# Optimization experiments

Hardware: AMD Instinct MI355X
Metric: run time of the kernel (lower is better)

The kernel has to match this reference:

```python
import jax, jax.numpy as jnp
import numpy as np

B = 8192
K = 40          # history blocks of 61
STATS = 383     # 99 base + 120 + 10 + 150 + 4 option dims
D = 165 + 61 * K + STATS  # 2988


def _mha(q, k, v, kpm, w_in, b_in, w_out, b_out, nh=4):
    """PyTorch nn.MultiheadAttention (batch_first) math. kpm: True = masked key."""
    Bq, Lq, E = q.shape
    hd = E // nh
    wq, wk, wv = jnp.split(w_in, 3, axis=0)
    bq, bk, bv = jnp.split(b_in, 3)
    qh = (q @ wq.T + bq).reshape(Bq, Lq, nh, hd).transpose(0, 2, 1, 3)
    kh = (k @ wk.T + bk).reshape(Bq, -1, nh, hd).transpose(0, 2, 1, 3)
    vh = (v @ wv.T + bv).reshape(Bq, -1, nh, hd).transpose(0, 2, 1, 3)
    s = jnp.einsum('bhqd,bhkd->bhqk', qh, kh) * jnp.float32(1.0 / np.sqrt(hd))
    if kpm is not None:
        s = jnp.where(kpm[:, None, None, :], jnp.float32(-1e9), s)
    a = jax.nn.softmax(s, axis=-1)
    o = jnp.einsum('bhqk,bhkd->bhqd', a, vh).transpose(0, 2, 1, 3).reshape(Bq, Lq, E)
    return o @ w_out.T + b_out


def _ln(x, g, b, eps=1e-5):
    m = x.mean(-1, keepdims=True)
    v = ((x - m) ** 2).mean(-1, keepdims=True)
    return (x - m) / jnp.sqrt(v + eps) * g + b


def setup_inputs() -> dict:
    key = jax.random.key(0)
    ks = iter(jax.random.split(key, 64))
    def p(shape, scale=0.02):
        return jax.random.normal(next(ks), shape, dtype=jnp.float32) * scale
    return {
        'obs': jax.random.normal(next(ks), (B, D), dtype=jnp.float32),
        'seat_team_vec': jax.random.normal(next(ks), (B, 6), dtype=jnp.float32),
        'card_emb': p((40, 32)),
        'w_cnt_hand': p((16, 3)), 'b_cnt_hand': p((16,)),
        'w_cnt_cap': p((16, 2)), 'b_cnt_cap': p((16,)),
        'h2t_win': p((96, 32)), 'h2t_bin': p((96,)), 'h2t_wout': p((32, 32)), 'h2t_bout': p((32,)),
        't2h_win': p((96, 32)), 't2h_bin': p((96,)), 't2h_wout': p((32, 32)), 't2h_bout': p((32,)),
        'w_merge': p((64, 224)), 'b_merge': p((64,)),
        'w_hproj': p((64, 61)), 'b_hproj': p((64,)),
        'pos_emb': p((40, 64)),
        'enc_win': p((192, 64)), 'enc_bin': p((192,)), 'enc_wout': p((64, 64)), 'enc_bout': p((64,)),
        'ln1_g': jnp.ones((64,), jnp.float32), 'ln1_b': jnp.zeros((64,), jnp.float32),
        'w_ff1': p((128, 64)), 'b_ff1': p((128,)),
        'w_ff2': p((64, 128)), 'b_ff2': p((64,)),
        'ln2_g': jnp.ones((64,), jnp.float32), 'ln2_b': jnp.zeros((64,), jnp.float32),
        'w_stats': p((64, STATS)), 'b_stats': p((64,)),
        'w_seat': p((32, 6)), 'b_seat': p((32,)),
        'w_comb': p((256, 224)), 'b_comb': p((256,)),
    }


def reference(obs, seat_team_vec, card_emb, w_cnt_hand, b_cnt_hand, w_cnt_cap, b_cnt_cap,
              h2t_win, h2t_bin, h2t_wout, h2t_bout, t2h_win, t2h_bin, t2h_wout, t2h_bout,
              w_merge, b_merge, w_hproj, b_hproj, pos_emb,
              enc_win, enc_bin, enc_wout, enc_bout, ln1_g, ln1_b,
              w_ff1, b_ff1, w_ff2, b_ff2, ln2_g, ln2_b,
              w_stats, b_stats, w_seat, b_seat, w_comb, b_comb):
    Bn = obs.shape[0]
    k = K  # static: decoded from D = 165 + 61*K + STATS
    hand_table = obs[:, :83]
    captured = obs[:, 83:165]
    history = obs[:, 165:165 + 61 * k]
    stats = obs[:, 165 + 61 * k:]

    hand_mask = hand_table[:, :40]
    other_counts = hand_table[:, 40:43]
    table_mask = hand_table[:, 43:83]

    hand_feat = hand_mask @ card_emb      # [B,32]
    table_feat = table_mask @ card_emb
    other_cnt_feat = jax.nn.relu(other_counts @ w_cnt_hand.T + b_cnt_hand)

    hand_present = hand_mask > 0.5
    table_present = table_mask > 0.5
    hand_seq = hand_mask[:, :, None] * card_emb    # [B,40,32]
    table_seq = table_mask[:, :, None] * card_emb

    # _safe_mha: rows whose keys are all padded produce zeros
    h2t = _mha(hand_seq, table_seq, table_seq, ~table_present, h2t_win, h2t_bin, h2t_wout, h2t_bout)
    h2t = jnp.where(table_present.any(axis=1)[:, None, None], h2t, jnp.float32(0.0))
    t2h = _mha(table_seq, hand_seq, hand_seq, ~hand_present, t2h_win, t2h_bin, t2h_wout, t2h_bout)
    t2h = jnp.where(hand_present.any(axis=1)[:, None, None], t2h, jnp.float32(0.0))

    def masked_mean(x, present):
        m = present[:, :, None].astype(x.dtype)
        return (x * m).sum(1) / jnp.maximum(m.sum(1), 1.0)
    hand_attn_feat = masked_mean(h2t, hand_present)
    table_attn_feat = masked_mean(t2h, table_present)

    cap0_feat = captured[:, :40] @ card_emb
    cap1_feat = captured[:, 40:80] @ card_emb
    cap_cnt_feat = jax.nn.relu(captured[:, 80:82] @ w_cnt_cap.T + b_cnt_cap)

    set_merged = jnp.concatenate([hand_feat, table_feat, cap0_feat, cap1_feat,
                                  hand_attn_feat, table_attn_feat,
                                  other_cnt_feat, cap_cnt_feat], axis=1)  # [B,224]
    set_feat = jax.nn.relu(set_merged @ w_merge.T + b_merge)              # [B,64]

    # 1-layer post-norm TransformerEncoder (eval mode, no dropout)
    hseq = history.reshape(Bn, k, 61) @ w_hproj.T + b_hproj + pos_emb[:k]  # [B,k,64]
    sa = _mha(hseq, hseq, hseq, None, enc_win, enc_bin, enc_wout, enc_bout)
    x = _ln(hseq + sa, ln1_g, ln1_b)
    ff = jax.nn.relu(x @ w_ff1.T + b_ff1) @ w_ff2.T + b_ff2
    x = _ln(x + ff, ln2_g, ln2_b)
    hist_feat = x.mean(axis=1)                                            # [B,64]

    stats_feat = jax.nn.relu(stats @ w_stats.T + b_stats)                 # [B,64]
    seat_feat = jax.nn.relu(seat_team_vec @ w_seat.T + b_seat)            # [B,32]

    combined = jnp.concatenate([set_feat, hist_feat, stats_feat, seat_feat], axis=1)  # [B,224]
    return jax.nn.relu(combined @ w_comb.T + b_comb)                      # [B,256]
```

## Files before the change

kernel.cpp:

```cpp
#include <hip/hip_runtime.h>

#define TPB 512

#define OFF_CV      0
#define OFF_POSB    2560
#define OFF_G       3840
#define OFF_U       10240
#define OFF_V       10560
#define OFF_CTB     10880
#define OFF_FRHP    10888
#define OFF_FRAG    14984
#define FR_QKV      0
#define FR_OUT      12288
#define FR_FF1      16384
#define FR_FF2      24576
#define OFF_ONES    47752
#define OFF_MERGE   48264
#define OFF_STATS   62600
#define OFF_COMB    74856
#define OFF_WO2     132200
#define WS_TOTAL    133224

#define SA_OFF    0
#define HISTH_OFF 10240
#define HISTL_OFF 16768
#define QPL_OFF   10240
#define KF_OFF    16384
#define KZ_OFF    22528
#define OH_OFF    10240
#define FF1P_OFF  10240
#define DH_OFF    23296
#define DL_OFF    30208
#define P_OFF     23296
#define YTAIL_OFF 36096
#define Z_OFF     37120
#define VF_OFF    37120
#define SHT_OFF   47360
#define SOM_OFF   48032
#define SSM_OFF   48544
#define SCB_OFF   49440
#define R12_OFF   50464
#define SCNT_OFF  52512
#define SMEM_BYTES 52520

typedef __attribute__((ext_vector_type(8))) short bf16x8;
typedef __attribute__((ext_vector_type(4))) float f32x4;

struct P {
  const float *obs, *seat, *ce, *wch, *bch, *wcc, *bcc,
    *h2t_win, *h2t_bin, *h2t_wout, *h2t_bout,
    *t2h_win, *t2h_bin, *t2h_wout, *t2h_bout,
    *w_merge, *b_merge, *w_hproj, *b_hproj, *pos,
    *enc_win, *enc_bin, *enc_wout, *enc_bout,
    *ln1_g, *ln1_b, *w_ff1, *b_ff1, *w_ff2, *b_ff2, *ln2_g, *ln2_b,
    *w_stats, *b_stats, *w_seat, *b_seat, *w_comb, *b_comb;
  const float* ws;
  float* out;
};

__device__ __host__ inline unsigned bfpack(float a, float b, int plane) {
  unsigned ua = __float_as_uint(a) & 0xFFFF0000u;
  unsigned ub = __float_as_uint(b) & 0xFFFF0000u;
  if (plane == 0) return (ua >> 16) | ub;
  float ra = a - __uint_as_float(ua), rb = b - __uint_as_float(ub);
  return (__float_as_uint(ra) >> 16) | (__float_as_uint(rb) & 0xFFFF0000u);
}

__device__ __host__ inline unsigned short bf16rne(float x) {
  unsigned u = __float_as_uint(x);
  return (unsigned short)((u + 0x7FFFu + ((u >> 16) & 1u)) >> 16);
}

__device__ __host__ inline unsigned packrne(float a, float b) {
  return (unsigned)bf16rne(a) | ((unsigned)bf16rne(b) << 16);
}

__device__ inline float bf_lo(unsigned u) { return __uint_as_float(u << 16); }
__device__ inline float bf_hi(unsigned u) { return __uint_as_float(u & 0xFFFF0000u); }

__device__ inline bf16x8 ld_b64x2(const char* pp) {
  bf16x8 v;
  *((uint2*)&v) = *(const uint2*)(pp);
  *(((uint2*)&v) + 1) = *(const uint2*)(pp + 8);
  return v;
}

#define CSCALE 0.35355339059327373f

__global__ void prep_kernel(P p, float* ws) {
  int t = blockIdx.x * blockDim.x + threadIdx.x;
  if (t >= WS_TOTAL) return;
  unsigned* wsu = (unsigned*)ws;
  if (t < OFF_POSB) {
    int a = t / 1280, rem = t - a * 1280;
    int i = rem >> 5, d = rem & 31;
    const float* win = a ? p.t2h_win : p.h2t_win;
    const float* wr = win + (64 + d) * 32;
    const float* cr = p.ce + i * 32;
    float acc = 0.f;
    #pragma unroll
    for (int j = 0; j < 32; ++j) acc += cr[j] * wr[j];
    ws[t] = acc;
  } else if (t < OFF_G) {
    int r = t - OFF_POSB; int i = r >> 5, u = r & 31;
    float a = p.b_hproj[2 * u] + p.pos[i * 64 + 2 * u];
    float b = p.b_hproj[2 * u + 1] + p.pos[i * 64 + 2 * u + 1];
    wsu[t] = packrne(a, b);
  } else if (t < OFF_U) {
    int r = t - OFF_G;
    int u = r % 20; int i = (r / 20) % 40; int h = (r / 800) & 3; int a = r / 3200;
    const float* win = a ? p.t2h_win : p.h2t_win;
    const float* cri = p.ce + i * 32;
    float g2[2];
    #pragma unroll
    for (int half = 0; half < 2; ++half) {
      int j = 2 * u + half;
      const float* crj = p.ce + j * 32;
      float g = 0.f;
      for (int e = 0; e < 8; ++e) {
        const float* wq = win + (h * 8 + e) * 32;
        const float* wk = win + (32 + h * 8 + e) * 32;
        float pq = 0.f, pk = 0.f;
        for (int m = 0; m < 32; ++m) { pq += cri[m] * wq[m]; pk += crj[m] * wk[m]; }
        g += pq * pk;
      }
      g2[half] = g * CSCALE;
    }
    wsu[t] = packrne(g2[0], g2[1]);
  } else if (t < OFF_V) {
    int r = t - OFF_U; int i = r % 40; int h = (r / 40) & 3; int a = r / 160;
    const float* win = a ? p.t2h_win : p.h2t_win;
    const float* bin = a ? p.t2h_bin : p.h2t_bin;
    const float* cri = p.ce + i * 32;
    float u = 0.f;
    for (int e = 0; e < 8; ++e) {
      const float* wq = win + (h * 8 + e) * 32;
      float pq = 0.f;
      for (int m = 0; m < 32; ++m) pq += cri[m] * wq[m];
      u += pq * bin[32 + h * 8 + e];
    }
    ws[t] = u * CSCALE;
  } else if (t < OFF_CTB) {
    int r = t - OFF_V; int j = r % 40; int h = (r / 40) & 3; int a = r / 160;
    const float* win = a ? p.t2h_win : p.h2t_win;
    const float* bin = a ? p.t2h_bin : p.h2t_bin;
    const float* crj = p.ce + j * 32;
    float v = 0.f;
    for (int e = 0; e < 8; ++e) {
      const float* wk = win + (32 + h * 8 + e) * 32;
      float pk = 0.f;
      for (int m = 0; m < 32; ++m) pk += crj[m] * wk[m];
      v += pk * bin[h * 8 + e];
    }
    ws[t] = v * CSCALE;
  } else if (t < OFF_FRHP) {
    int r = t - OFF_CTB; int h = r & 3; int a = r >> 2;
    const float* bin = a ? p.t2h_bin : p.h2t_bin;
    float c = 0.f;
    for (int e = 0; e < 8; ++e) c += bin[h * 8 + e] * bin[32 + h * 8 + e];
    ws[t] = c * CSCALE;
  } else if (t < OFF_FRAG) {
    int r = t - OFF_FRHP;
    int plane = r >> 11; r &= 2047; int kt = r >> 10; r &= 1023;
    int nt = r >> 8; r &= 255; int lane = r >> 2; int u = r & 3;
    int k = kt * 32 + (lane >> 4) * 8 + u * 2;
    int n = nt * 16 + (lane & 15);
    float a = (k < 61) ? p.w_hproj[n * 61 + k] : 0.f;
    float b = (k + 1 < 61) ? p.w_hproj[n * 61 + k + 1] : 0.f;
    wsu[t] = bfpack(a, b, plane);
  } else if (t < OFF_ONES) {
    int r = t - OFF_FRAG;
    int plane, kt, nt, lane, u;
    const float* src; int ldk;
    if (r < FR_OUT) {
      plane = r / 6144; r %= 6144; kt = r / 3072; r %= 3072;
      nt = r >> 8; r &= 255; lane = r >> 2; u = r & 3;
      src = p.enc_win; ldk = 64;
    } else if (r < FR_FF1) {
      r -= FR_OUT; plane = r >> 11; r &= 2047; kt = r >> 10; r &= 1023;
      nt = r >> 8; r &= 255; lane = r >> 2; u = r & 3;
      src = p.enc_wout; ldk = 64;
    } else if (r < FR_FF2) {
      r -= FR_FF1; plane = r >> 12; r &= 4095; kt = r >> 11; r &= 2047;
      nt = r >> 8; r &= 255; lane = r >> 2; u = r & 3;
      src = p.w_ff1; ldk = 64;
    } else {
      r -= FR_FF2; plane = r >> 12; r &= 4095; kt = r >> 10; r &= 1023;
      nt = r >> 8; r &= 255; lane = r >> 2; u = r & 3;
      src = p.w_ff2; ldk = 128;
    }
    int k = kt * 32 + (lane >> 4) * 8 + u * 2;
    int n = nt * 16 + (lane & 15);
    float a = src[n * ldk + k], b = src[n * ldk + k + 1];
    wsu[t] = bfpack(a, b, plane);
  } else if (t < OFF_MERGE) {
    int r = t - OFF_ONES;
    int kt = r >> 8, rr = r & 255;
    int lane = rr >> 2, u = rr & 3;
    int k = kt * 32 + (lane >> 4) * 8 + u * 2;
    wsu[t] = ((k < 40) ? 0x00003F80u : 0u) | ((k + 1 < 40) ? 0x3F800000u : 0u);
  } else if (t < OFF_STATS) {
    int r = t - OFF_MERGE; int j = r >> 6, d = r & 63;
    ws[t] = p.w_merge[d * 224 + j];
  } else if (t < OFF_COMB) {
    int r = t - OFF_STATS;
    int j = r >> 5, pp = r & 31;
    wsu[t] = packrne(p.w_stats[(2 * pp) * 383 + j], p.w_stats[(2 * pp + 1) * 383 + j]);
  } else if (t < OFF_WO2) {
    int r = t - OFF_COMB;
    int jq = r >> 10, rem = r & 1023;
    int n = rem >> 2, c = rem & 3;
    ws[t] = p.w_comb[n * 224 + jq * 4 + c];
  } else {
    int r = t - OFF_WO2; int a = r >> 9; int rr = r & 511;
    int e = rr >> 4, u = rr & 15;
    const float* src = a ? p.t2h_wout : p.h2t_wout;
    wsu[t] = packrne(src[(2 * u) * 32 + e], src[(2 * u + 1) * 32 + e]);
  }
}

#define FMA4(acc, a4, w0, w1, w2, w3)                                   \
  acc.x += a4.x * w0.x + a4.y * w1.x + a4.z * w2.x + a4.w * w3.x;       \
  acc.y += a4.x * w0.y + a4.y * w1.y + a4.z * w2.y + a4.w * w3.y;       \
  acc.z += a4.x * w0.z + a4.y * w1.z + a4.z * w2.z + a4.w * w3.z;       \
  acc.w += a4.x * w0.w + a4.y * w1.w + a4.z * w2.w + a4.w * w3.w;

#define MFMA16(acc, a, b) acc = __builtin_amdgcn_mfma_f32_16x16x32_bf16(a, b, acc, 0, 0, 0)

__global__ __launch_bounds__(TPB, 3) void enc_row(P p) {
  const int row = blockIdx.x;
  const int tid = threadIdx.x;
  const int lane = tid & 63, wq = tid >> 6;
  const int lane15 = lane & 15, lg = lane >> 4;

  __shared__ unsigned smem_u[SMEM_BYTES / 4];
  char* smem = (char*)smem_u;
  float* sA   = (float*)(smem + SA_OFF);
  float* sZ   = (float*)(smem + Z_OFF);
  float* s_ht = (float*)(smem + SHT_OFF);
  float* s_om = (float*)(smem + SOM_OFF);
  float* s_sm = (float*)(smem + SSM_OFF);
  float* s_cb = (float*)(smem + SCB_OFF);
  float* s_r12 = (float*)(smem + R12_OFF);
  int*   s_cnt = (int*)(smem + SCNT_OFF);

  const float* orow = p.obs + (size_t)row * 2988;
  const float* ws = p.ws;
  const unsigned* wsu = (const unsigned*)ws;

  if (tid < 165) s_ht[tid] = orow[tid];
  if (tid < 256) ((unsigned*)(smem + YTAIL_OFF))[tid] = 0u;
  if (tid < 256) {
    int feat = tid >> 6, q = tid & 63;
    int d = q >> 1, jh = q & 1;
    const int offs[4] = {0, 43, 83, 123};
    const int dsts[4] = {0, 32, 64, 96};
    int off = offs[feat];
    float a = 0.f;
    for (int j = jh * 20; j < jh * 20 + 20; ++j)
      a += orow[off + j] * p.ce[j * 32 + d];
    float other = __shfl_xor(a, 1, 64);
    if (jh == 0) s_sm[dsts[feat] + d] = a + other;
  } else if (tid < 272) {
    int d = tid - 256;
    float a = p.bch[d];
    for (int j = 0; j < 3; ++j) a += orow[40 + j] * p.wch[d * 3 + j];
    s_sm[192 + d] = fmaxf(a, 0.f);
  } else if (tid < 288) {
    int d = tid - 272;
    float a = p.bcc[d];
    for (int j = 0; j < 2; ++j) a += orow[163 + j] * p.wcc[d * 2 + j];
    s_sm[208 + d] = fmaxf(a, 0.f);
  } else if (tid < 352) {
    s_sm[128 + tid - 288] = 0.f;
  } else if (tid < 480) {
    s_om[tid - 352] = 0.f;
  } else if (tid == 480) {
    int c = 0; for (int i = 0; i < 40; ++i) c += (orow[i] > 0.5f);
    s_cnt[0] = c;
  } else if (tid == 481) {
    int c = 0; for (int i = 0; i < 40; ++i) c += (orow[43 + i] > 0.5f);
    s_cnt[1] = c;
  }
  if (tid < 64) s_cb[128 + tid] = p.b_stats[tid];
  else if (tid < 128) s_cb[tid - 64] = p.b_merge[tid - 64];
  else if (tid < 256) s_r12[tid - 128] = 0.f;
  for (int m = tid; m < 2560; m += TPB) {
    int i = m >> 6, j = m & 63;
    float val = (j < 61) ? orow[165 + i * 61 + j] : 0.f;
    unsigned hb = __float_as_uint(val) & 0xFFFF0000u;
    *(unsigned short*)(smem + HISTH_OFF + i * 136 + j * 2) = (unsigned short)(hb >> 16);
    float rr = val - __uint_as_float(hb);
    *(unsigned short*)(smem + HISTL_OFF + i * 136 + j * 2) =
        (unsigned short)(__float_as_uint(rr) >> 16);
  }
  for (int m = tid; m < 2560; m += TPB) sZ[m] = ws[OFF_CV + m];
  __syncthreads();
  #define OB(i) s_ht[i]

  for (int t = wq; t < 12; t += 8) {
    int rt = t % 3, nt = t / 3;
    int n = nt * 16 + lane15;
    int arow = rt * 16 + lane15;
    f32x4 acc;
    #pragma unroll
    for (int r = 0; r < 4; ++r) {
      int i = rt * 16 + lg * 4 + r;
      if (i < 40) {
        unsigned pb = wsu[OFF_POSB + i * 32 + (n >> 1)];
        acc[r] = (n & 1) ? bf_hi(pb) : bf_lo(pb);
      } else acc[r] = 0.f;
    }
    #pragma unroll
    for (int kt = 0; kt < 2; ++kt) {
      int kb = kt * 32 + lg * 8;
      bf16x8 aH = ld_b64x2(smem + HISTH_OFF + arow * 136 + kb * 2);
      bf16x8 aL = ld_b64x2(smem + HISTL_OFF + arow * 136 + kb * 2);
      bf16x8 bH = *(const bf16x8*)(wsu + OFF_FRHP + kt * 1024 + nt * 256 + lane * 4);
      bf16x8 bL = *(const bf16x8*)(wsu + OFF_FRHP + 2048 + kt * 1024 + nt * 256 + lane * 4);
      MFMA16(acc, aH, bH); MFMA16(acc, aH, bL); MFMA16(acc, aL, bH);
    }
    #pragma unroll
    for (int r = 0; r < 4; ++r) {
      int i = rt * 16 + lg * 4 + r;
      if (i < 40) {
        sA[i * 64 + n] = acc[r];
        unsigned hb = __float_as_uint(acc[r]) & 0xFFFF0000u;
        *(unsigned short*)(smem + DH_OFF + i * 144 + n * 2) = (unsigned short)(hb >> 16);
        float rr = acc[r] - __uint_as_float(hb);
        *(unsigned short*)(smem + DL_OFF + i * 144 + n * 2) =
            (unsigned short)(__float_as_uint(rr) >> 16);
      }
    }
  }
  if (tid < 320) {
    int a = tid / 160, r = tid - a * 160;
    int h = r / 40, i = r - h * 40;
    int qoff = a ? 43 : 0, koff = a ? 0 : 43;
    float qm = OB(qoff + i);
    const unsigned* Gp = wsu + OFF_G + ((a * 4 + h) * 40 + i) * 20;
    const float* vp = ws + OFF_V + (a * 4 + h) * 40;
    const float* Cv = sZ + a * 1280;
    const float* bin = a ? p.t2h_bin : p.h2t_bin;
    float base = ws[OFF_CTB + a * 4 + h] + qm * ws[OFF_U + (a * 4 + h) * 40 + i];
    const int e0 = h * 8;
    float den = 0.f;
    float o0 = 0.f, o1 = 0.f, o2 = 0.f, o3 = 0.f;
    float o4 = 0.f, o5 = 0.f, o6 = 0.f, o7 = 0.f;
    for (int j = 0; j < 40; ++j) {
      float km = OB(koff + j);
      if (km > 0.5f) {
        unsigned g2 = Gp[j >> 1];
        float gj = (j & 1) ? bf_hi(g2) : bf_lo(g2);
        float s = fmaf(km, fmaf(qm, gj, vp[j]), base);
        float pj = __expf(s);
        den += pj;
        float pk = pj * km;
        float4 v0 = *(const float4*)(Cv + j * 32 + e0);
        float4 v1 = *(const float4*)(Cv + j * 32 + e0 + 4);
        o0 += pk * v0.x; o1 += pk * v0.y; o2 += pk * v0.z; o3 += pk * v0.w;
        o4 += pk * v1.x; o5 += pk * v1.y; o6 += pk * v1.z; o7 += pk * v1.w;
      }
    }
    if (qm > 0.5f) {
      float inv = 1.f / den;
      float4 bv0 = *(const float4*)(bin + 64 + e0);
      float4 bv1 = *(const float4*)(bin + 64 + e0 + 4);
      float* om = s_om + (i & 1) * 64 + a * 32 + e0;
      atomicAdd(&om[0], o0 * inv + bv0.x);
      atomicAdd(&om[1], o1 * inv + bv0.y);
      atomicAdd(&om[2], o2 * inv + bv0.z);
      atomicAdd(&om[3], o3 * inv + bv0.w);
      atomicAdd(&om[4], o4 * inv + bv1.x);
      atomicAdd(&om[5], o5 * inv + bv1.y);
      atomicAdd(&om[6], o6 * inv + bv1.z);
      atomicAdd(&om[7], o7 * inv + bv1.w);
    }
  } else {
    int r = tid - 320;
    int c = r >> 4, d0 = (r & 15) << 2;
    int j0 = c << 5, j1 = (c == 11) ? 383 : j0 + 32;
    const float* st = orow + 2605;
    const unsigned* wt = wsu + OFF_STATS + (d0 >> 1);
    float x0 = 0.f, x1 = 0.f, x2 = 0.f, x3 = 0.f;
    for (int j = j0; j < j1; ++j) {
      float a0 = st[j];
      unsigned u0 = wt[j * 32], u1 = wt[j * 32 + 1];
      x0 += a0 * bf_lo(u0); x1 += a0 * bf_hi(u0);
      x2 += a0 * bf_lo(u1); x3 += a0 * bf_hi(u1);
    }
    float* bank = (c & 1) ? s_r12 : (s_cb + 128);
    atomicAdd(&bank[d0 + 0], x0);
    atomicAdd(&bank[d0 + 1], x1);
    atomicAdd(&bank[d0 + 2], x2);
    atomicAdd(&bank[d0 + 3], x3);
  }
  __syncthreads();

  for (int t = wq; t < 36; t += 8) {
    int rt = t % 3, nt = t / 3;
    int n = nt * 16 + lane15;
    int arow = rt * 16 + lane15;
    float bia = p.enc_bin[n];
    f32x4 acc = {bia, bia, bia, bia};
    #pragma unroll
    for (int kt = 0; kt < 2; ++kt) {
      int kb = kt * 32 + lg * 8;
      bf16x8 aH = *(const bf16x8*)(smem + DH_OFF + arow * 144 + kb * 2);
      bf16x8 aL = *(const bf16x8*)(smem + DL_OFF + arow * 144 + kb * 2);
      bf16x8 bH = *(const bf16x8*)(wsu + OFF_FRAG + FR_QKV + kt * 3072 + nt * 256 + lane * 4);
      bf16x8 bL = *(const bf16x8*)(wsu + OFF_FRAG + FR_QKV + 6144 + kt * 3072 + nt * 256 + lane * 4);
      MFMA16(acc, aH, bH); MFMA16(acc, aH, bL); MFMA16(acc, aL, bH);
    }
    if (nt < 4) {
      #pragma unroll
      for (int r = 0; r < 4; ++r) {
        int i = rt * 16 + lg * 4 + r;
        if (i < 40)
          *(unsigned short*)(smem + QPL_OFF + ((nt * 48 + i) * 16 + lane15) * 2) =
              bf16rne(acc[r]);
      }
    } else if (nt < 8) {
      int h = nt - 4, e = lane15;
      int lp = (e >> 3) << 4, us = e & 7;
      #pragma unroll
      for (int r = 0; r < 4; ++r) {
        int j = rt * 16 + lg * 4 + r;
        if (j < 40) {
          int lanep = lp + (j & 15);
          *(unsigned short*)(smem + KF_OFF +
              (((h * 3 + (j >> 4)) * 32 + lanep) * 8 + us) * 2) = bf16rne(acc[r]);
        }
      }
    } else {
      int h = nt - 8, e = lane15;
      #pragma unroll
      for (int r = 0; r < 4; ++r) {
        int j = rt * 16 + lg * 4 + r;
        if (j < 40) {
          int kt = j >> 5, k_ = j & 31;
          int lanep = ((k_ >> 3) << 4) | e;
          *(unsigned short*)(smem + VF_OFF +
              (((h * 2 + kt) * 64 + lanep) * 8 + (k_ & 7)) * 2) = bf16rne(acc[r]);
        }
      }
    }
  }
  if (tid < 128) ((unsigned*)(smem + KZ_OFF))[tid] = 0u;
  for (int m = tid; m < 768; m += TPB) {
    int h = m / 192, rem = m - h * 192;
    ((unsigned*)(smem + VF_OFF))[(h * 2 + 1) * 256 + 64 + rem] = 0u;
  }
  if (tid >= 448 && tid < 480) {
    int r = tid - 448;
    int a = r >> 4, q = r & 15;
    int d0 = (q >> 1) << 2, eh = q & 1;
    int ch = s_cnt[0], ct = s_cnt[1];
    if (ch > 0 && ct > 0) {
      float ic = 1.f / (float)(a ? ct : ch);
      const unsigned* wt = wsu + OFF_WO2 + a * 512 + (d0 >> 1);
      float4 v = make_float4(0.f, 0.f, 0.f, 0.f);
      if (eh == 0) v = *(const float4*)((a ? p.t2h_bout : p.h2t_bout) + d0);
      for (int e = eh * 16; e < eh * 16 + 16; ++e) {
        float oe = (s_om[a * 32 + e] + s_om[64 + a * 32 + e]) * ic;
        unsigned w01 = wt[e * 16], w23 = wt[e * 16 + 1];
        v.x += oe * bf_lo(w01); v.y += oe * bf_hi(w01);
        v.z += oe * bf_lo(w23); v.w += oe * bf_hi(w23);
      }
      atomicAdd(&s_sm[128 + a * 32 + d0 + 0], v.x);
      atomicAdd(&s_sm[128 + a * 32 + d0 + 1], v.y);
      atomicAdd(&s_sm[128 + a * 32 + d0 + 2], v.z);
      atomicAdd(&s_sm[128 + a * 32 + d0 + 3], v.w);
    }
  }
  __syncthreads();

  for (int t = wq; t < 36; t += 8) {
    int h = t / 9, rr = t % 9;
    int rt = rr / 3, nt = rr % 3;
    int arow = rt * 16 + lane15;
    f32x4 acc = {0.f, 0.f, 0.f, 0.f};
    bf16x8 aH = *(const bf16x8*)(smem + QPL_OFF + ((h * 48 + arow) * 16 + (lg & 1) * 8) * 2);
    int boff = (lane < 32) ? (KF_OFF + (((h * 3 + nt) * 32 + lane) * 8) * 2)
                           : (KZ_OFF + ((lane & 31) * 8) * 2);
    bf16x8 bH = *(const bf16x8*)(smem + boff);
    MFMA16(acc, aH, bH);
    int j = nt * 16 + lane15;
    if (j < 40) {
      #pragma unroll
      for (int r = 0; r < 4; ++r) {
        int i = rt * 16 + lg * 4 + r;
        if (i < 40)
          *(unsigned short*)(smem + P_OFF + h * 3200 + i * 80 + j * 2) =
              bf16rne(__expf(acc[r] * 0.25f));
      }
    }
  }
  __syncthreads();

  {
    bf16x8 ones0 = *(const bf16x8*)(wsu + OFF_ONES + lane * 4);
    bf16x8 ones1 = *(const bf16x8*)(wsu + OFF_ONES + 256 + lane * 4);
    for (int t = wq; t < 12; t += 8) {
      int h = t / 3, rt = t % 3;
      int arow = rt * 16 + lane15;
      const char* pb = smem + P_OFF + h * 3200 + arow * 80;
      bf16x8 a0 = *(const bf16x8*)(pb + lg * 16);
      bf16x8 a1 = {0, 0, 0, 0, 0, 0, 0, 0};
      if (lg == 0) a1 = *(const bf16x8*)(pb + 64);
      bf16x8 v0 = *(const bf16x8*)(smem + VF_OFF + ((h * 2 + 0) * 64 + lane) * 16);
      bf16x8 v1 = *(const bf16x8*)(smem + VF_OFF + ((h * 2 + 1) * 64 + lane) * 16);
      f32x4 accV = {0.f, 0.f, 0.f, 0.f}, accD = {0.f, 0.f, 0.f, 0.f};
      MFMA16(accV, a0, v0); MFMA16(accV, a1, v1);
      MFMA16(accD, a0, ones0); MFMA16(accD, a1, ones1);
      #pragma unroll
      for (int r = 0; r < 4; ++r) {
        int i = rt * 16 + lg * 4 + r;
        if (i < 40) {
          float o = accV[r] / accD[r];
          *(unsigned short*)(smem + OH_OFF + (i * 72 + h * 16 + lane15) * 2) =
              bf16rne(o);
        }
      }
    }
  }
  if (tid >= 256 && tid < 384) {
    int r = tid - 256;
    int d0 = (r & 15) << 2, jc = r >> 4;
    const float* wt = ws + OFF_MERGE + d0;
    float4 acc = make_float4(0.f, 0.f, 0.f, 0.f);
    int j0 = jc * 28;
    for (int j = j0; j < j0 + 28; j += 4) {
      float4 a4 = *(const float4*)(s_sm + j);
      float4 w0 = *(const float4*)(wt + j * 64);
      float4 w1 = *(const float4*)(wt + (j + 1) * 64);
      float4 w2 = *(const float4*)(wt + (j + 2) * 64);
      float4 w3 = *(const float4*)(wt + (j + 3) * 64);
      FMA4(acc, a4, w0, w1, w2, w3);
    }
    float* bank = (jc & 1) ? (s_r12 + 64) : s_cb;
    atomicAdd(&bank[d0 + 0], acc.x);
    atomicAdd(&bank[d0 + 1], acc.y);
    atomicAdd(&bank[d0 + 2], acc.z);
    atomicAdd(&bank[d0 + 3], acc.w);
  }
  __syncthreads();

  for (int t = wq; t < 12; t += 8) {
    int rt = t % 3, nt = t / 3;
    int n = nt * 16 + lane15;
    int arow = rt * 16 + lane15;
    f32x4 acc;
    #pragma unroll
    for (int r = 0; r < 4; ++r) {
      int i = rt * 16 + lg * 4 + r;
      acc[r] = p.enc_bout[n] + ((i < 40) ? sA[i * 64 + n] : 0.f);
    }
    #pragma unroll
    for (int kt = 0; kt < 2; ++kt) {
      int kb = kt * 32 + lg * 8;
      bf16x8 aH = *(const bf16x8*)(smem + OH_OFF + arow * 144 + kb * 2);
      bf16x8 bH = *(const bf16x8*)(wsu + OFF_FRAG + FR_OUT + kt * 1024 + nt * 256 + lane * 4);
      bf16x8 bL = *(const bf16x8*)(wsu + OFF_FRAG + FR_OUT + 2048 + kt * 1024 + nt * 256 + lane * 4);
      MFMA16(acc, aH, bH); MFMA16(acc, aH, bL);
    }
    #pragma unroll
    for (int r = 0; r < 4; ++r) {
      int i = rt * 16 + lg * 4 + r;
      if (i < 40) sZ[i * 64 + n] = acc[r];
    }
  }
  __syncthreads();

  {
    float g = p.ln1_g[lane], b = p.ln1_b[lane];
    for (int i = wq; i < 40; i += 8) {
      float x = sZ[(i << 6) + lane];
      float s = x;
      #pragma unroll
      for (int off = 32; off; off >>= 1) s += __shfl_xor(s, off, 64);
      float m = s * 0.015625f;
      float xm = x - m;
      float v = xm * xm;
      #pragma unroll
      for (int off = 32; off; off >>= 1) v += __shfl_xor(v, off, 64);
      float rs = rsqrtf(v * 0.015625f + 1e-5f);
      float val = xm * rs * g + b;
      sA[(i << 6) + lane] = val;
      unsigned hb = __float_as_uint(val) & 0xFFFF0000u;
      *(unsigned short*)(smem + DH_OFF + i * 144 + lane * 2) = (unsigned short)(hb >> 16);
      float rr = val - __uint_as_float(hb);
      *(unsigned short*)(smem + DL_OFF + i * 144 + lane * 2) =
          (unsigned short)(__float_as_uint(rr) >> 16);
    }
  }
  __syncthreads();

  for (int t = wq; t < 24; t += 8) {
    int rt = t % 3, nt = t / 3;
    int n = nt * 16 + lane15;
    int arow = rt * 16 + lane15;
    float bia = p.b_ff1[n];
    f32x4 acc = {bia, bia, bia, bia};
    #pragma unroll
    for (int kt = 0; kt < 2; ++kt) {
      int kb = kt * 32 + lg * 8;
      bf16x8 aH = *(const bf16x8*)(smem + DH_OFF + arow * 144 + kb * 2);
      bf16x8 aL = *(const bf16x8*)(smem + DL_OFF + arow * 144 + kb * 2);
      bf16x8 bH = *(const bf16x8*)(wsu + OFF_FRAG + FR_FF1 + kt * 2048 + nt * 256 + lane * 4);
      bf16x8 bL = *(const bf16x8*)(wsu + OFF_FRAG + FR_FF1 + 4096 + kt * 2048 + nt * 256 + lane * 4);
      MFMA16(acc, aH, bH); MFMA16(acc, aH, bL); MFMA16(acc, aL, bH);
    }
    #pragma unroll
    for (int r = 0; r < 4; ++r) {
      int i = rt * 16 + lg * 4 + r;
      float v = fmaxf(acc[r], 0.f);
      *(unsigned short*)(smem + FF1P_OFF + i * 272 + n * 2) = bf16rne(v);
    }
  }
  __syncthreads();

  for (int t = wq; t < 12; t += 8) {
    int rt = t % 3, nt = t / 3;
    int n = nt * 16 + lane15;
    int arow = rt * 16 + lane15;
    f32x4 acc;
    #pragma unroll
    for (int r = 0; r < 4; ++r) {
      int i = rt * 16 + lg * 4 + r;
      acc[r] = p.b_ff2[n] + ((i < 40) ? sA[i * 64 + n] : 0.f);
    }
    #pragma unroll
    for (int kt = 0; kt < 4; ++kt) {
      int kb = kt * 32 + lg * 8;
      bf16x8 aH = *(const bf16x8*)(smem + FF1P_OFF + arow * 272 + kb * 2);
      bf16x8 bH = *(const bf16x8*)(wsu + OFF_FRAG + FR_FF2 + kt * 1024 + nt * 256 + lane * 4);
      bf16x8 bL = *(const bf16x8*)(wsu + OFF_FRAG + FR_FF2 + 4096 + kt * 1024 + nt * 256 + lane * 4);
      MFMA16(acc, aH, bH); MFMA16(acc, aH, bL);
    }
    #pragma unroll
    for (int r = 0; r < 4; ++r) {
      int i = rt * 16 + lg * 4 + r;
      if (i < 40) sZ[i * 64 + n] = acc[r];
    }
  }
  __syncthreads();

  {
    float g = p.ln2_g[lane], b = p.ln2_b[lane];
    for (int i = wq; i < 40; i += 8) {
      float x = sZ[(i << 6) + lane];
      float s = x;
      #pragma unroll
      for (int off = 32; off; off >>= 1) s += __shfl_xor(s, off, 64);
      float m = s * 0.015625f;
      float xm = x - m;
      float v = xm * xm;
      #pragma unroll
      for (int off = 32; off; off >>= 1) v += __shfl_xor(v, off, 64);
      float rs = rsqrtf(v * 0.015625f + 1e-5f);
      sA[(i << 6) + lane] = xm * rs * g + b;
    }
  }
  __syncthreads();

  if (tid < 64) {
    float a = 0.f;
    for (int i = 0; i < 40; ++i) a += sA[(i << 6) + tid];
    s_cb[64 + tid] = a * 0.025f;
    s_cb[128 + tid] = fmaxf(s_cb[128 + tid] + s_r12[tid], 0.f);
    s_cb[tid] = fmaxf(s_cb[tid] + s_r12[64 + tid], 0.f);
  } else if (tid < 96) {
    int d = tid - 64;
    const float* sv = p.seat + (size_t)row * 6;
    float acc = p.b_seat[d];
    for (int j = 0; j < 6; ++j) acc += sv[j] * p.w_seat[d * 6 + j];
    s_cb[192 + d] = fmaxf(acc, 0.f);
  }
  __syncthreads();

  {
    int n = tid & 255, half = tid >> 8;
    const float* wt = ws + OFF_COMB + n * 4;
    float acc = half ? 0.f : p.b_comb[n];
    int jq0 = half * 28;
    for (int jq = jq0; jq < jq0 + 28; ++jq) {
      float4 a4 = *(const float4*)(s_cb + jq * 4);
      float4 w = *(const float4*)(wt + jq * 1024);
      acc += a4.x * w.x + a4.y * w.y + a4.z * w.z + a4.w * w.w;
    }
    s_r12[half * 256 + n] = acc;
  }
  __syncthreads();
  if (tid < 256)
    p.out[(size_t)row * 256 + tid] = fmaxf(s_r12[tid] + s_r12[256 + tid], 0.f);
  #undef OB
}

extern "C" void kernel_launch(void* const* d_in, const int* in_sizes, int n_in,
                              void* d_out, int out_size, void* d_ws, size_t ws_size,
                              hipStream_t stream) {
  typedef const float* F;
  P p;
  p.obs      = (F)d_in[0];
  p.seat     = (F)d_in[1];
  p.ce       = (F)d_in[2];
  p.wch      = (F)d_in[3];
  p.bch      = (F)d_in[4];
  p.wcc      = (F)d_in[5];
  p.bcc      = (F)d_in[6];
  p.h2t_win  = (F)d_in[7];
  p.h2t_bin  = (F)d_in[8];
  p.h2t_wout = (F)d_in[9];
  p.h2t_bout = (F)d_in[10];
  p.t2h_win  = (F)d_in[11];
  p.t2h_bin  = (F)d_in[12];
  p.t2h_wout = (F)d_in[13];
  p.t2h_bout = (F)d_in[14];
  p.w_merge  = (F)d_in[15];
  p.b_merge  = (F)d_in[16];
  p.w_hproj  = (F)d_in[17];
  p.b_hproj  = (F)d_in[18];
  p.pos      = (F)d_in[19];
  p.enc_win  = (F)d_in[20];
  p.enc_bin  = (F)d_in[21];
  p.enc_wout = (F)d_in[22];
  p.enc_bout = (F)d_in[23];
  p.ln1_g    = (F)d_in[24];
  p.ln1_b    = (F)d_in[25];
  p.w_ff1    = (F)d_in[26];
  p.b_ff1    = (F)d_in[27];
  p.w_ff2    = (F)d_in[28];
  p.b_ff2    = (F)d_in[29];
  p.ln2_g    = (F)d_in[30];
  p.ln2_b    = (F)d_in[31];
  p.w_stats  = (F)d_in[32];
  p.b_stats  = (F)d_in[33];
  p.w_seat   = (F)d_in[34];
  p.b_seat   = (F)d_in[35];
  p.w_comb   = (F)d_in[36];
  p.b_comb   = (F)d_in[37];
  p.ws  = (const float*)d_ws;
  p.out = (float*)d_out;

  const int Bn = in_sizes[0] / 2988;
  hipLaunchKernelGGL(prep_kernel, dim3((WS_TOTAL + 255) / 256), dim3(256), 0, stream,
                     p, (float*)d_ws);
  hipLaunchKernelGGL(enc_row, dim3(Bn), dim3(TPB), 0, stream, p);
}
```

Measured before the change: 825.4 us.

## Shrink shared memory with bf16 activations to fit four blocks per CU

Stores the residual/LN activation buffers sA and sZ as bf16 instead of fp32. It also reads the Cv table straight from global memory instead of staging it in LDS, and drops the zero-padding buffers (YTAIL, KZ) by zeroing the B operand in registers. Shared memory shrinks from about 52KB to about 41KB and launch bounds rise to 4 blocks per CU, aiming for higher occupancy. The cost is lower precision on the residual path and LayerNorm outputs, plus extra global reads for Cv.

```diff
diff --git a/kernel.cpp b/kernel.cpp
--- a/kernel.cpp
+++ b/kernel.cpp
@@ -22,26 +22,25 @@
 #define WS_TOTAL    133224
 
 #define SA_OFF    0
-#define HISTH_OFF 10240
-#define HISTL_OFF 16768
-#define QPL_OFF   10240
-#define KF_OFF    16384
-#define KZ_OFF    22528
-#define OH_OFF    10240
-#define FF1P_OFF  10240
-#define DH_OFF    23296
-#define DL_OFF    30208
-#define P_OFF     23296
-#define YTAIL_OFF 36096
-#define Z_OFF     37120
-#define VF_OFF    37120
-#define SHT_OFF   47360
-#define SOM_OFF   48032
-#define SSM_OFF   48544
-#define SCB_OFF   49440
-#define R12_OFF   50464
-#define SCNT_OFF  52512
-#define SMEM_BYTES 52520
+#define HISTH_OFF 5120
+#define HISTL_OFF 10560
+#define QPL_OFF   5120
+#define KF_OFF    10240
+#define OH_OFF    5120
+#define FF1P_OFF  5120
+#define DH_OFF    16384
+#define DL_OFF    22144
+#define P_OFF     16384
+#define Z_OFF     29184
+#define VF_OFF    29184
+#define BNK_OFF   37376
+#define SHT_OFF   37888
+#define SOM_OFF   38548
+#define SSM_OFF   39060
+#define SCB_OFF   39956
+#define SCNT_OFF  40852
+#define R12_OFF   37888
+#define SMEM_BYTES 40860
 
 typedef __attribute__((ext_vector_type(8))) short bf16x8;
 typedef __attribute__((ext_vector_type(4))) float f32x4;
@@ -77,6 +76,9 @@
 
 __device__ inline float bf_lo(unsigned u) { return __uint_as_float(u << 16); }
 __device__ inline float bf_hi(unsigned u) { return __uint_as_float(u & 0xFFFF0000u); }
+__device__ inline float bfus(unsigned short u) {
+  return __uint_as_float(((unsigned)u) << 16);
+}
 
 __device__ inline bf16x8 ld_b64x2(const char* pp) {
   bf16x8 v;
@@ -227,7 +229,7 @@
 
 #define MFMA16(acc, a, b) acc = __builtin_amdgcn_mfma_f32_16x16x32_bf16(a, b, acc, 0, 0, 0)
 
-__global__ __launch_bounds__(TPB, 3) void enc_row(P p) {
+__global__ __launch_bounds__(TPB, 4) void enc_row(P p) {
   const int row = blockIdx.x;
   const int tid = threadIdx.x;
   const int lane = tid & 63, wq = tid >> 6;
@@ -235,12 +237,13 @@
 
   __shared__ unsigned smem_u[SMEM_BYTES / 4];
   char* smem = (char*)smem_u;
-  float* sA   = (float*)(smem + SA_OFF);
-  float* sZ   = (float*)(smem + Z_OFF);
-  float* s_ht = (float*)(smem + SHT_OFF);
-  float* s_om = (float*)(smem + SOM_OFF);
-  float* s_sm = (float*)(smem + SSM_OFF);
-  float* s_cb = (float*)(smem + SCB_OFF);
+  unsigned short* sAu = (unsigned short*)(smem + SA_OFF);
+  unsigned short* sZu = (unsigned short*)(smem + Z_OFF);
+  float* s_bnk = (float*)(smem + BNK_OFF);
+  float* s_ht  = (float*)(smem + SHT_OFF);
+  float* s_om  = (float*)(smem + SOM_OFF);
+  float* s_sm  = (float*)(smem + SSM_OFF);
+  float* s_cb  = (float*)(smem + SCB_OFF);
   float* s_r12 = (float*)(smem + R12_OFF);
   int*   s_cnt = (int*)(smem + SCNT_OFF);
 
@@ -249,7 +252,6 @@
   const unsigned* wsu = (const unsigned*)ws;
 
   if (tid < 165) s_ht[tid] = orow[tid];
-  if (tid < 256) ((unsigned*)(smem + YTAIL_OFF))[tid] = 0u;
   if (tid < 256) {
     int feat = tid >> 6, q = tid & 63;
     int d = q >> 1, jh = q & 1;
@@ -284,7 +286,7 @@
   }
   if (tid < 64) s_cb[128 + tid] = p.b_stats[tid];
   else if (tid < 128) s_cb[tid - 64] = p.b_merge[tid - 64];
-  else if (tid < 256) s_r12[tid - 128] = 0.f;
+  else if (tid < 256) s_bnk[tid - 128] = 0.f;
   for (int m = tid; m < 2560; m += TPB) {
     int i = m >> 6, j = m & 63;
     float val = (j < 61) ? orow[165 + i * 61 + j] : 0.f;
@@ -294,7 +296,6 @@
     *(unsigned short*)(smem + HISTL_OFF + i * 136 + j * 2) =
         (unsigned short)(__float_as_uint(rr) >> 16);
   }
-  for (int m = tid; m < 2560; m += TPB) sZ[m] = ws[OFF_CV + m];
   __syncthreads();
   #define OB(i) s_ht[i]
 
@@ -324,7 +325,7 @@
     for (int r = 0; r < 4; ++r) {
       int i = rt * 16 + lg * 4 + r;
       if (i < 40) {
-        sA[i * 64 + n] = acc[r];
+        sAu[i * 64 + n] = bf16rne(acc[r]);
         unsigned hb = __float_as_uint(acc[r]) & 0xFFFF0000u;
         *(unsigned short*)(smem + DH_OFF + i * 144 + n * 2) = (unsigned short)(hb >> 16);
         float rr = acc[r] - __uint_as_float(hb);
@@ -340,7 +341,7 @@
     float qm = OB(qoff + i);
     const unsigned* Gp = wsu + OFF_G + ((a * 4 + h) * 40 + i) * 20;
     const float* vp = ws + OFF_V + (a * 4 + h) * 40;
-    const float* Cv = sZ + a * 1280;
+    const float* Cv = ws + OFF_CV + a * 1280;
     const float* bin = a ? p.t2h_bin : p.h2t_bin;
     float base = ws[OFF_CTB + a * 4 + h] + qm * ws[OFF_U + (a * 4 + h) * 40 + i];
     const int e0 = h * 8;
@@ -389,7 +390,7 @@
       x0 += a0 * bf_lo(u0); x1 += a0 * bf_hi(u0);
       x2 += a0 * bf_lo(u1); x3 += a0 * bf_hi(u1);
     }
-    float* bank = (c & 1) ? s_r12 : (s_cb + 128);
+    float* bank = (c & 1) ? s_bnk : (s_cb + 128);
     atomicAdd(&bank[d0 + 0], x0);
     atomicAdd(&bank[d0 + 1], x1);
     atomicAdd(&bank[d0 + 2], x2);
@@ -417,7 +418,7 @@
       for (int r = 0; r < 4; ++r) {
         int i = rt * 16 + lg * 4 + r;
         if (i < 40)
-          *(unsigned short*)(smem + QPL_OFF + ((nt * 48 + i) * 16 + lane15) * 2) =
+          *(unsigned short*)(smem + QPL_OFF + ((nt * 40 + i) * 16 + lane15) * 2) =
               bf16rne(acc[r]);
       }
     } else if (nt < 8) {
@@ -446,7 +447,6 @@
       }
     }
   }
-  if (tid < 128) ((unsigned*)(smem + KZ_OFF))[tid] = 0u;
   for (int m = tid; m < 768; m += TPB) {
     int h = m / 192, rem = m - h * 192;
     ((unsigned*)(smem + VF_OFF))[(h * 2 + 1) * 256 + 64 + rem] = 0u;
@@ -480,10 +480,10 @@
     int rt = rr / 3, nt = rr % 3;
     int arow = rt * 16 + lane15;
     f32x4 acc = {0.f, 0.f, 0.f, 0.f};
-    bf16x8 aH = *(const bf16x8*)(smem + QPL_OFF + ((h * 48 + arow) * 16 + (lg & 1) * 8) * 2);
-    int boff = (lane < 32) ? (KF_OFF + (((h * 3 + nt) * 32 + lane) * 8) * 2)
-                           : (KZ_OFF + ((lane & 31) * 8) * 2);
-    bf16x8 bH = *(const bf16x8*)(smem + boff);
+    bf16x8 aH = *(const bf16x8*)(smem + QPL_OFF + ((h * 40 + arow) * 16 + (lg & 1) * 8) * 2);
+    bf16x8 bH = {0, 0, 0, 0, 0, 0, 0, 0};
+    if (lane < 32)
+      bH = *(const bf16x8*)(smem + KF_OFF + (((h * 3 + nt) * 32 + lane) * 8) * 2);
     MFMA16(acc, aH, bH);
     int j = nt * 16 + lane15;
     if (j < 40) {
@@ -538,7 +538,7 @@
       float4 w3 = *(const float4*)(wt + (j + 3) * 64);
       FMA4(acc, a4, w0, w1, w2, w3);
     }
-    float* bank = (jc & 1) ? (s_r12 + 64) : s_cb;
+    float* bank = (jc & 1) ? (s_bnk + 64) : s_cb;
     atomicAdd(&bank[d0 + 0], acc.x);
     atomicAdd(&bank[d0 + 1], acc.y);
     atomicAdd(&bank[d0 + 2], acc.z);
@@ -554,7 +554,7 @@
     #pragma unroll
     for (int r = 0; r < 4; ++r) {
       int i = rt * 16 + lg * 4 + r;
-      acc[r] = p.enc_bout[n] + ((i < 40) ? sA[i * 64 + n] : 0.f);
+      acc[r] = p.enc_bout[n] + ((i < 40) ? bfus(sAu[i * 64 + n]) : 0.f);
     }
     #pragma unroll
     for (int kt = 0; kt < 2; ++kt) {
@@ -567,7 +567,7 @@
     #pragma unroll
     for (int r = 0; r < 4; ++r) {
       int i = rt * 16 + lg * 4 + r;
-      if (i < 40) sZ[i * 64 + n] = acc[r];
+      if (i < 40) sZu[i * 64 + n] = bf16rne(acc[r]);
     }
   }
   __syncthreads();
@@ -575,7 +575,7 @@
   {
     float g = p.ln1_g[lane], b = p.ln1_b[lane];
     for (int i = wq; i < 40; i += 8) {
-      float x = sZ[(i << 6) + lane];
+      float x = bfus(sZu[(i << 6) + lane]);
       float s = x;
       #pragma unroll
       for (int off = 32; off; off >>= 1) s += __shfl_xor(s, off, 64);
@@ -586,7 +586,7 @@
       for (int off = 32; off; off >>= 1) v += __shfl_xor(v, off, 64);
       float rs = rsqrtf(v * 0.015625f + 1e-5f);
       float val = xm * rs * g + b;
-      sA[(i << 6) + lane] = val;
+      sAu[(i << 6) + lane] = bf16rne(val);
       unsigned hb = __float_as_uint(val) & 0xFFFF0000u;
       *(unsigned short*)(smem + DH_OFF + i * 144 + lane * 2) = (unsigned short)(hb >> 16);
       float rr = val - __uint_as_float(hb);
@@ -614,8 +614,10 @@
     #pragma unroll
     for (int r = 0; r < 4; ++r) {
       int i = rt * 16 + lg * 4 + r;
-      float v = fmaxf(acc[r], 0.f);
-      *(unsigned short*)(smem + FF1P_OFF + i * 272 + n * 2) = bf16rne(v);
+      if (i < 40) {
+        float v = fmaxf(acc[r], 0.f);
+        *(unsigned short*)(smem + FF1P_OFF + i * 272 + n * 2) = bf16rne(v);
+      }
     }
   }
   __syncthreads();
@@ -628,7 +630,7 @@
     #pragma unroll
     for (int r = 0; r < 4; ++r) {
       int i = rt * 16 + lg * 4 + r;
-      acc[r] = p.b_ff2[n] + ((i < 40) ? sA[i * 64 + n] : 0.f);
+      acc[r] = p.b_ff2[n] + ((i < 40) ? bfus(sAu[i * 64 + n]) : 0.f);
     }
     #pragma unroll
     for (int kt = 0; kt < 4; ++kt) {
@@ -641,7 +643,7 @@
     #pragma unroll
     for (int r = 0; r < 4; ++r) {
       int i = rt * 16 + lg * 4 + r;
-      if (i < 40) sZ[i * 64 + n] = acc[r];
+      if (i < 40) sZu[i * 64 + n] = bf16rne(acc[r]);
     }
   }
   __syncthreads();
@@ -649,7 +651,7 @@
   {
     float g = p.ln2_g[lane], b = p.ln2_b[lane];
     for (int i = wq; i < 40; i += 8) {
-      float x = sZ[(i << 6) + lane];
+      float x = bfus(sZu[(i << 6) + lane]);
       float s = x;
       #pragma unroll
       for (int off = 32; off; off >>= 1) s += __shfl_xor(s, off, 64);
@@ -659,17 +661,17 @@
       #pragma unroll
       for (int off = 32; off; off >>= 1) v += __shfl_xor(v, off, 64);
       float rs = rsqrtf(v * 0.015625f + 1e-5f);
-      sA[(i << 6) + lane] = xm * rs * g + b;
+      sAu[(i << 6) + lane] = bf16rne(xm * rs * g + b);
     }
   }
   __syncthreads();
 
   if (tid < 64) {
     float a = 0.f;
-    for (int i = 0; i < 40; ++i) a += sA[(i << 6) + tid];
+    for (int i = 0; i < 40; ++i) a += bfus(sAu[(i << 6) + tid]);
     s_cb[64 + tid] = a * 0.025f;
-    s_cb[128 + tid] = fmaxf(s_cb[128 + tid] + s_r12[tid], 0.f);
-    s_cb[tid] = fmaxf(s_cb[tid] + s_r12[64 + tid], 0.f);
+    s_cb[128 + tid] = fmaxf(s_cb[128 + tid] + s_bnk[tid], 0.f);
+    s_cb[tid] = fmaxf(s_cb[tid] + s_bnk[64 + tid], 0.f);
   } else if (tid < 96) {
     int d = tid - 64;
     const float* sv = p.seat + (size_t)row * 6;
```

Result: slower. 966.5 us (+17.1%).
